# Optimization experiments

Hardware: AMD Instinct MI355X
Metric: run time of the kernel (lower is better)

Reference implementation:

```python
import jax, jax.numpy as jnp
import numpy as np


def setup_inputs() -> dict:
    key = jax.random.key(0)
    ks = jax.random.split(key, 5)
    B, S, D = 4, 2048, 1024
    x = jax.random.normal(ks[0], (B, S, D), dtype=jnp.float32)
    wq = jax.random.normal(ks[1], (D, D), dtype=jnp.float32) * (D ** -0.5)
    wk = jax.random.normal(ks[2], (D, D), dtype=jnp.float32) * (D ** -0.5)
    wv = jax.random.normal(ks[3], (D, D), dtype=jnp.float32) * (D ** -0.5)
    wo = jax.random.normal(ks[4], (D, D), dtype=jnp.float32) * (D ** -0.5)
    return {"x": x, "wq": wq, "wk": wk, "wv": wv, "wo": wo, "n_heads": 16}


def reference(x, wq, wk, wv, wo, n_heads):
    B, S, D = x.shape
    hd = D // n_heads
    # projections (module computes x @ w.T)
    q = (x @ wq.T).reshape(B, S, n_heads, hd).transpose(0, 2, 1, 3)  # b h s d
    k = (x @ wk.T).reshape(B, S, n_heads, hd).transpose(0, 2, 1, 3)
    v = (x @ wv.T).reshape(B, S, n_heads, hd).transpose(0, 2, 1, 3)
    # NOTE: module scales by sqrt(d_model), not sqrt(head_dim)
    scores = jnp.einsum("bhqd,bhkd->bhqk", q, k) / jnp.sqrt(jnp.float32(D))
    # module bug preserved: masked_fill(mask == 0, -1e9) with mask = triu(diag=1)
    # fills positions where mask is False (lower triangle incl. diagonal).
    triu_mask = jnp.triu(jnp.ones((S, S), dtype=bool), k=1)  # True strictly above diag
    scores = jnp.where(triu_mask, scores, jnp.float32(-1e9))
    attn = jax.nn.softmax(scores, axis=-1)
    out = jnp.einsum("bhqk,bhkd->bhqd", attn, v)  # b h s d
    out = out.transpose(0, 2, 1, 3).reshape(B, S, D)
    return out @ wo.T
```

## Files before the change

### kernel.cpp

```cpp
#include <hip/hip_runtime.h>
#include <hip/hip_bf16.h>

typedef __attribute__((ext_vector_type(8))) short short8;
typedef __attribute__((ext_vector_type(4))) short bfx4;
typedef __attribute__((ext_vector_type(4))) float floatx4;
typedef __attribute__((ext_vector_type(4))) __fp16 h4_t;
typedef __attribute__((ext_vector_type(2))) __fp16 h2_t;
typedef __attribute__((ext_vector_type(8))) __fp16 h8_t;

#define BATCH 4
#define SEQ 2048
#define D_MODEL 1024
#define NH 16
#define HD 64
#define ELEMS 8388608
#define WELEMS 1048576

__device__ __forceinline__ unsigned short f2bf(float f) {
    union { float f; unsigned u; } x; x.f = f;
    unsigned r = x.u + 0x7FFFu + ((x.u >> 16) & 1u);
    return (unsigned short)(r >> 16);
}
__device__ __forceinline__ unsigned short f2h(float f) {
    union { __fp16 h; unsigned short u; } x;
    x.h = (__fp16)f;
    return x.u;
}

#if __has_builtin(__builtin_amdgcn_exp2f)
__device__ __forceinline__ float fexp2(float x) { return __builtin_amdgcn_exp2f(x); }
#else
__device__ __forceinline__ float fexp2(float x) { return exp2f(x); }
#endif

__device__ __forceinline__ void gll16(const void* g, const void* l) {
    __builtin_amdgcn_global_load_lds(
        (const __attribute__((address_space(1))) void*)g,
        (__attribute__((address_space(3))) void*)l,
        16, 0, 0);
}


__global__ __launch_bounds__(256)
void cvt_kernel(const float* __restrict__ x,  const float* __restrict__ wq,
                const float* __restrict__ wk, const float* __restrict__ wv,
                const float* __restrict__ wo,
                unsigned short* __restrict__ xbf,
                unsigned short* __restrict__ wqkv,
                unsigned short* __restrict__ wobf)
{
    size_t idx = ((size_t)blockIdx.x * 256 + threadIdx.x) * 8;
    const float* src; unsigned short* dst; size_t off;
    if (idx < (size_t)ELEMS)                    { src = x;  dst = xbf;             off = idx; }
    else if (idx < (size_t)ELEMS + WELEMS)      { src = wq; dst = wqkv;            off = idx - ELEMS; }
    else if (idx < (size_t)ELEMS + 2 * WELEMS)  { src = wk; dst = wqkv + WELEMS;   off = idx - ELEMS - WELEMS; }
    else if (idx < (size_t)ELEMS + 3 * WELEMS)  { src = wv; dst = wqkv + 2*WELEMS; off = idx - ELEMS - 2*WELEMS; }
    else                                        { src = wo; dst = wobf;            off = idx - ELEMS - 3*WELEMS; }
    floatx4 a = *(const floatx4*)(src + off);
    floatx4 b = *(const floatx4*)(src + off + 4);
    short8 v;
#pragma unroll
    for (int d = 0; d < 4; d++) { v[d] = (short)f2bf(a[d]); v[4+d] = (short)f2bf(b[d]); }
    *(short8*)(dst + off) = v;
}

__global__ __launch_bounds__(256, 2)
void gemm_qkv3_kernel(const unsigned short* __restrict__ A,
                      const unsigned short* __restrict__ B,
                      unsigned short* __restrict__ Qb,
                      unsigned short* __restrict__ Kb,
                      unsigned short* __restrict__ Vb)
{
    __shared__ __align__(16) unsigned short As[128 * 64];
    __shared__ __align__(16) unsigned short Bs[128 * 64];

    const int t = threadIdx.x;
    const int wave = t >> 6, lane = t & 63;
    const int lm = lane & 15, lq = lane >> 4;
    const int wrow = (wave >> 1) * 64, wcol = (wave & 1) * 64;
    const int m0 = blockIdx.x * 128, n0 = blockIdx.y * 128;
    const int lrow = lane >> 3, lg = lane & 7;
    const int gsw = lg ^ lrow;

    floatx4 acc[4][4] = {};

    for (int k0 = 0; k0 < 1024; k0 += 64) {
        __syncthreads();
#pragma unroll
        for (int i = 0; i < 4; i++) {
            int rows8 = wave * 32 + i * 8;
            gll16(A + (size_t)(m0 + rows8 + lrow) * 1024 + k0 + gsw * 8, As + rows8 * 64);
            gll16(B + (size_t)(n0 + rows8 + lrow) * 1024 + k0 + gsw * 8, Bs + rows8 * 64);
        }
        __syncthreads();

#pragma unroll
        for (int c = 0; c < 2; c++) {
            short8 af[4], bfr[4];
#pragma unroll
            for (int i = 0; i < 4; i++) {
                int ra = wrow + i * 16 + lm;
                int g = c * 4 + lq;
                af[i] = *(const short8*)(As + (ra * 8 + (g ^ (ra & 7))) * 8);
            }
#pragma unroll
            for (int j = 0; j < 4; j++) {
                int rb = wcol + j * 16 + lm;
                int g = c * 4 + lq;
                bfr[j] = *(const short8*)(Bs + (rb * 8 + (g ^ (rb & 7))) * 8);
            }
#pragma unroll
            for (int i = 0; i < 4; i++)
#pragma unroll
                for (int j = 0; j < 4; j++)
                    acc[i][j] = __builtin_amdgcn_mfma_f32_16x16x32_bf16(
                        af[i], bfr[j], acc[i][j], 0, 0, 0);
        }
    }

    const int z = n0 >> 10;
#pragma unroll
    for (int i = 0; i < 4; i++)
#pragma unroll
        for (int j = 0; j < 4; j++)
#pragma unroll
            for (int r = 0; r < 4; r++) {
                int gm = m0 + wrow + i * 16 + lq * 4 + r;
                int gn = n0 + wcol + j * 16 + lm;
                int nl = gn & 1023, h = nl >> 6, d = nl & 63;
                int b = gm >> 11, s = gm & 2047;
                float v = acc[i][j][r];
                size_t bh = (size_t)(b * NH + h);
                if (z == 0)      Qb[(bh * SEQ + s) * HD + d] = f2bf(v);
                else if (z == 1) Kb[(bh * SEQ + s) * HD + d] = f2bf(v);
                else             Vb[(bh * HD + d) * SEQ + s] = f2h(v);
            }
}

__global__ __launch_bounds__(256, 2)
void gemm_out3_kernel(const unsigned short* __restrict__ A,
                      const unsigned short* __restrict__ B,
                      float* __restrict__ Out)
{
    __shared__ __align__(16) unsigned short As[128 * 64];
    __shared__ __align__(16) unsigned short Bs[128 * 64];

    const int t = threadIdx.x;
    const int wave = t >> 6, lane = t & 63;
    const int lm = lane & 15, lq = lane >> 4;
    const int wrow = (wave >> 1) * 64, wcol = (wave & 1) * 64;
    const int m0 = blockIdx.x * 128, n0 = blockIdx.y * 128;
    const int lrow = lane >> 3, lg = lane & 7;
    const int gsw = lg ^ lrow;

    floatx4 acc[4][4] = {};

    for (int k0 = 0; k0 < 1024; k0 += 64) {
        __syncthreads();
#pragma unroll
        for (int i = 0; i < 4; i++) {
            int rows8 = wave * 32 + i * 8;
            gll16(A + (size_t)(m0 + rows8 + lrow) * 1024 + k0 + gsw * 8, As + rows8 * 64);
            gll16(B + (size_t)(n0 + rows8 + lrow) * 1024 + k0 + gsw * 8, Bs + rows8 * 64);
        }
        __syncthreads();

#pragma unroll
        for (int c = 0; c < 2; c++) {
            short8 af[4], bfr[4];
#pragma unroll
            for (int i = 0; i < 4; i++) {
                int ra = wrow + i * 16 + lm;
                int g = c * 4 + lq;
                af[i] = *(const short8*)(As + (ra * 8 + (g ^ (ra & 7))) * 8);
            }
#pragma unroll
            for (int j = 0; j < 4; j++) {
                int rb = wcol + j * 16 + lm;
                int g = c * 4 + lq;
                bfr[j] = *(const short8*)(Bs + (rb * 8 + (g ^ (rb & 7))) * 8);
            }
#pragma unroll
            for (int i = 0; i < 4; i++)
#pragma unroll
                for (int j = 0; j < 4; j++)
                    acc[i][j] = __builtin_amdgcn_mfma_f32_16x16x32_bf16(
                        af[i], bfr[j], acc[i][j], 0, 0, 0);
        }
    }

#pragma unroll
    for (int i = 0; i < 4; i++)
#pragma unroll
        for (int j = 0; j < 4; j++)
#pragma unroll
            for (int r = 0; r < 4; r++) {
                int gm = m0 + wrow + i * 16 + lq * 4 + r;
                int gn = n0 + wcol + j * 16 + lm;
                Out[(size_t)gm * D_MODEL + gn] = acc[i][j][r];
            }
}

#define PROCESS_Q(QI, BQ, ACC, LACC, DOMASK, KT)                               \
    do {                                                                       \
        _Pragma("unroll")                                                      \
        for (int jt = 0; jt < 8; jt++) {                                       \
            floatx4 sc = {};                                                   \
            _Pragma("unroll")                                                  \
            for (int c = 0; c < 2; c++) {                                      \
                int row_ = jt * 16 + lm;                                       \
                int g_ = c * 4 + lq;                                           \
                short8 kf = *(const short8*)(Ks + (row_ * 8 + (g_ ^ (row_ & 7))) * 8); \
                sc = __builtin_amdgcn_mfma_f32_16x16x32_bf16(kf, BQ[c], sc, 0, 0, 0); \
            }                                                                  \
            if (DOMASK) {                                                      \
                _Pragma("unroll")                                              \
                for (int r = 0; r < 4; r++) {                                  \
                    int kj = (KT) * 128 + jt * 16 + lq * 4 + r;                \
                    if (!(kj > (QI))) sc[r] = -3.2e10f;                        \
                }                                                              \
            }                                                                  \
            float p0 = fexp2(sc[0] * kA), p1 = fexp2(sc[1] * kA);              \
            float p2 = fexp2(sc[2] * kA), p3 = fexp2(sc[3] * kA);              \
            LACC += (p0 + p1) + (p2 + p3);                                     \
            h2_t a01 = __builtin_amdgcn_cvt_pkrtz(p0, p1);                     \
            h2_t a23 = __builtin_amdgcn_cvt_pkrtz(p2, p3);                     \
            h4_t pf;                                                           \
            pf[0] = a01[0]; pf[1] = a01[1]; pf[2] = a23[0]; pf[3] = a23[1];    \
            _Pragma("unroll")                                                  \
            for (int jd = 0; jd < 4; jd++) {                                   \
                int rowv_ = jd * 16 + lm;                                      \
                int g16_ = jt * 2 + (lq >> 1);                                 \
                int slot_ = rowv_ * 16 + (g16_ ^ lm);                          \
                h4_t vf = *(const h4_t*)((const __fp16*)Vs + slot_ * 8 + (lq & 1) * 4); \
                ACC[jd] = __builtin_amdgcn_mfma_f32_16x16x16f16(vf, pf, ACC[jd], 0, 0, 0); \
            }                                                                  \
        }                                                                      \
    } while (0)

__global__ __launch_bounds__(256, 2)
void attn5_kernel(const unsigned short* __restrict__ Q,
                  const unsigned short* __restrict__ K,
                  const unsigned short* __restrict__ V,
                  unsigned short* __restrict__ O)
{
    __shared__ __align__(16) unsigned short Ks[128 * 64];
    __shared__ __align__(16) unsigned short Vs[64 * 128];

    const int t = threadIdx.x;
    const int wave = t >> 6, lane = t & 63;
    const int lm = lane & 15, lq = lane >> 4;
    const int bh = blockIdx.y;
    const int jlo = blockIdx.x, jhi = 31 - jlo;
    const int qlo = jlo * 64 + wave * 16 + lm;
    const int qhi = jhi * 64 + wave * 16 + lm;

    const unsigned short* Qh = Q + (size_t)bh * SEQ * HD;
    const unsigned short* Kh = K + (size_t)bh * SEQ * HD;
    const unsigned short* Vh = V + (size_t)bh * HD * SEQ;

    short8 bq_lo[2], bq_hi[2];
    bq_lo[0] = *(const short8*)(Qh + (size_t)qlo * HD + lq * 8);
    bq_lo[1] = *(const short8*)(Qh + (size_t)qlo * HD + 32 + lq * 8);
    bq_hi[0] = *(const short8*)(Qh + (size_t)qhi * HD + lq * 8);
    bq_hi[1] = *(const short8*)(Qh + (size_t)qhi * HD + 32 + lq * 8);

    floatx4 acc_lo[4] = {}, acc_hi[4] = {};
    float l_lo = 0.f, l_hi = 0.f;
    const float kA = 0.04508422002778011f;

    const int lrow = lane >> 3, lg = lane & 7;
    const int kt_min = jlo >> 1;
    const int kthi_min = 15 - kt_min;

    for (int kt = 15; kt >= kt_min; kt--) {
        __syncthreads();
#pragma unroll
        for (int i = 0; i < 4; i++) {
            int rows8 = wave * 32 + i * 8;
            gll16(Kh + (size_t)(kt * 128 + rows8 + lrow) * HD + (lg ^ lrow) * 8,
                  Ks + rows8 * 64);
        }
#pragma unroll
        for (int i = 0; i < 4; i++) {
            int rows4 = wave * 16 + i * 4;
            int row = rows4 + (lane >> 4);
            int g = (lane & 15) ^ (row & 15);
            gll16(Vh + (size_t)row * SEQ + kt * 128 + g * 8, Vs + rows4 * 128);
        }
        __syncthreads();

        PROCESS_Q(qlo, bq_lo, acc_lo, l_lo, (kt == kt_min), kt);
        if (kt >= kthi_min)
            PROCESS_Q(qhi, bq_hi, acc_hi, l_hi, (kt == kthi_min), kt);
    }

    const int b = bh >> 4, h = bh & 15;
    {
        float l = l_lo;
        l += __shfl_xor(l, 16); l += __shfl_xor(l, 32);
        float inv = 1.0f / l;
#pragma unroll
        for (int jd = 0; jd < 4; jd++) {
            bfx4 o;
#pragma unroll
            for (int r = 0; r < 4; r++) o[r] = (short)f2bf(acc_lo[jd][r] * inv);
            *(bfx4*)(O + (size_t)(b * SEQ + qlo) * D_MODEL + h * HD + jd * 16 + lq * 4) = o;
        }
    }
    {
        float l = l_hi;
        l += __shfl_xor(l, 16); l += __shfl_xor(l, 32);
        float inv = 1.0f / l;
#pragma unroll
        for (int jd = 0; jd < 4; jd++) {
            bfx4 o;
#pragma unroll
            for (int r = 0; r < 4; r++) o[r] = (short)f2bf(acc_hi[jd][r] * inv);
            *(bfx4*)(O + (size_t)(b * SEQ + qhi) * D_MODEL + h * HD + jd * 16 + lq * 4) = o;
        }
    }
}

__global__ __launch_bounds__(256, 2)
void row2047_kernel(const unsigned short* __restrict__ V,
                    unsigned short* __restrict__ O)
{
    __shared__ float red[256];
    const int bh = blockIdx.x;
    const int b = bh >> 4, h = bh & 15;
    const int t = threadIdx.x;
    const int d = t & 63, seg = t >> 6;
    const __fp16* Vh = (const __fp16*)V + (size_t)bh * HD * SEQ + (size_t)d * SEQ + seg * 512;
    float s = 0.f;
    for (int i = 0; i < 512; i += 8) {
        h8_t v = *(const h8_t*)(Vh + i);
#pragma unroll
        for (int j = 0; j < 8; j++) s += (float)v[j];
    }
    red[t] = s;
    __syncthreads();
    if (seg == 0) {
        float tot = red[d] + red[64 + d] + red[128 + d] + red[192 + d];
        O[(size_t)(b * SEQ + 2047) * D_MODEL + h * HD + d] = f2bf(tot * (1.f / 2048.f));
    }
}

__global__ __launch_bounds__(256, 2)
void gemm_qkv_kernel(const float* __restrict__ A,
                     const float* __restrict__ W0,
                     const float* __restrict__ W1,
                     const float* __restrict__ W2,
                     unsigned short* __restrict__ O0,
                     unsigned short* __restrict__ O1,
                     unsigned short* __restrict__ O2)
{
    const int K = 1024;
    const float* W;
    unsigned short* Out;
    if (blockIdx.z == 0)      { W = W0; Out = O0; }
    else if (blockIdx.z == 1) { W = W1; Out = O1; }
    else                      { W = W2; Out = O2; }

    __shared__ __align__(16) unsigned short As[128 * 64];
    __shared__ __align__(16) unsigned short Bs[128 * 64];

    const int t = threadIdx.x;
    const int wave = t >> 6, lane = t & 63;
    const int lm = lane & 15, lq = lane >> 4;
    const int wrow = (wave >> 1) * 64, wcol = (wave & 1) * 64;
    const int m0 = blockIdx.x * 128, n0 = blockIdx.y * 128;

    floatx4 acc[4][4] = {};

    for (int k0 = 0; k0 < K; k0 += 64) {
        __syncthreads();
#pragma unroll
        for (int rr = 0; rr < 4; rr++) {
            int p = rr * 256 + t;
            int row = p >> 3, g = p & 7;
            const float* pa = A + (size_t)(m0 + row) * K + k0 + g * 8;
            const float* pw = W + (size_t)(n0 + row) * K + k0 + g * 8;
            floatx4 a0 = *(const floatx4*)pa, a1 = *(const floatx4*)(pa + 4);
            floatx4 w0 = *(const floatx4*)pw, w1 = *(const floatx4*)(pw + 4);
            short8 va, vb;
#pragma unroll
            for (int d = 0; d < 4; d++) {
                va[d]     = (short)f2bf(a0[d]);
                va[4 + d] = (short)f2bf(a1[d]);
                vb[d]     = (short)f2bf(w0[d]);
                vb[4 + d] = (short)f2bf(w1[d]);
            }
            int dst = row * 8 + (g ^ (row & 7));
            *(short8*)(As + dst * 8) = va;
            *(short8*)(Bs + dst * 8) = vb;
        }
        __syncthreads();

        short8 af[4][2], bf[4][2];
#pragma unroll
        for (int i = 0; i < 4; i++)
#pragma unroll
            for (int c = 0; c < 2; c++) {
                int ra = wrow + i * 16 + lm;
                int rb = wcol + i * 16 + lm;
                int g = c * 4 + lq;
                af[i][c] = *(const short8*)(As + (ra * 8 + (g ^ (ra & 7))) * 8);
                bf[i][c] = *(const short8*)(Bs + (rb * 8 + (g ^ (rb & 7))) * 8);
            }
#pragma unroll
        for (int i = 0; i < 4; i++)
#pragma unroll
            for (int j = 0; j < 4; j++)
#pragma unroll
                for (int c = 0; c < 2; c++)
                    acc[i][j] = __builtin_amdgcn_mfma_f32_16x16x32_bf16(
                        af[i][c], bf[j][c], acc[i][j], 0, 0, 0);
    }

    const int zi = blockIdx.z;
#pragma unroll
    for (int i = 0; i < 4; i++)
#pragma unroll
        for (int j = 0; j < 4; j++)
#pragma unroll
            for (int r = 0; r < 4; r++) {
                int gm = m0 + wrow + i * 16 + lq * 4 + r;
                int gn = n0 + wcol + j * 16 + lm;
                int b = gm >> 11, s = gm & 2047;
                int h = gn >> 6, d = gn & 63;
                if (zi == 2) {
                    Out[((size_t)(b * NH + h) * HD + d) * SEQ + s] = f2h(acc[i][j][r]);
                } else {
                    Out[((size_t)(b * NH + h) * SEQ + s) * HD + d] = f2bf(acc[i][j][r]);
                }
            }
}

__global__ __launch_bounds__(256, 2)
void gemm_out_kernel(const unsigned short* __restrict__ Abf,
                     const float* __restrict__ W,
                     float* __restrict__ Out)
{
    const int K = 1024;
    __shared__ __align__(16) unsigned short As[128 * 64];
    __shared__ __align__(16) unsigned short Bs[128 * 64];

    const int t = threadIdx.x;
    const int wave = t >> 6, lane = t & 63;
    const int lm = lane & 15, lq = lane >> 4;
    const int wrow = (wave >> 1) * 64, wcol = (wave & 1) * 64;
    const int m0 = blockIdx.x * 128, n0 = blockIdx.y * 128;

    floatx4 acc[4][4] = {};

    for (int k0 = 0; k0 < K; k0 += 64) {
        __syncthreads();
#pragma unroll
        for (int rr = 0; rr < 4; rr++) {
            int p = rr * 256 + t;
            int row = p >> 3, g = p & 7;
            short8 va = *(const short8*)(Abf + (size_t)(m0 + row) * K + k0 + g * 8);
            const float* pw = W + (size_t)(n0 + row) * K + k0 + g * 8;
            floatx4 w0 = *(const floatx4*)pw, w1 = *(const floatx4*)(pw + 4);
            short8 vb;
#pragma unroll
            for (int d = 0; d < 4; d++) {
                vb[d]     = (short)f2bf(w0[d]);
                vb[4 + d] = (short)f2bf(w1[d]);
            }
            int dst = row * 8 + (g ^ (row & 7));
            *(short8*)(As + dst * 8) = va;
            *(short8*)(Bs + dst * 8) = vb;
        }
        __syncthreads();

        short8 af[4][2], bf[4][2];
#pragma unroll
        for (int i = 0; i < 4; i++)
#pragma unroll
            for (int c = 0; c < 2; c++) {
                int ra = wrow + i * 16 + lm;
                int rb = wcol + i * 16 + lm;
                int g = c * 4 + lq;
                af[i][c] = *(const short8*)(As + (ra * 8 + (g ^ (ra & 7))) * 8);
                bf[i][c] = *(const short8*)(Bs + (rb * 8 + (g ^ (rb & 7))) * 8);
            }
#pragma unroll
        for (int i = 0; i < 4; i++)
#pragma unroll
            for (int j = 0; j < 4; j++)
#pragma unroll
                for (int c = 0; c < 2; c++)
                    acc[i][j] = __builtin_amdgcn_mfma_f32_16x16x32_bf16(
                        af[i][c], bf[j][c], acc[i][j], 0, 0, 0);
    }

#pragma unroll
    for (int i = 0; i < 4; i++)
#pragma unroll
        for (int j = 0; j < 4; j++)
#pragma unroll
            for (int r = 0; r < 4; r++) {
                int gm = m0 + wrow + i * 16 + lq * 4 + r;
                int gn = n0 + wcol + j * 16 + lm;
                Out[(size_t)gm * D_MODEL + gn] = acc[i][j][r];
            }
}

extern "C" void kernel_launch(void* const* d_in, const int* in_sizes, int n_in,
                              void* d_out, int out_size, void* d_ws, size_t ws_size,
                              hipStream_t stream) {
    const float* x  = (const float*)d_in[0];
    const float* wq = (const float*)d_in[1];
    const float* wk = (const float*)d_in[2];
    const float* wv = (const float*)d_in[3];
    const float* wo = (const float*)d_in[4];

    unsigned short* ws = (unsigned short*)d_ws;
    const bool fast = ws_size >= (size_t)36 * 1024 * 1024 * 2;

    if (fast) {
        unsigned short* xbf  = ws;
        unsigned short* wqkv = ws + (size_t)ELEMS;
        unsigned short* wobf = ws + (size_t)ELEMS + 3 * WELEMS;
        unsigned short* Qb   = ws + (size_t)ELEMS + 4 * WELEMS;
        unsigned short* Kb   = Qb + ELEMS;
        unsigned short* Vb   = Kb + ELEMS;
        unsigned short* Ob   = xbf;

        cvt_kernel<<<6144, 256, 0, stream>>>(x, wq, wk, wv, wo, xbf, wqkv, wobf);
        gemm_qkv3_kernel<<<dim3(64, 24), 256, 0, stream>>>(xbf, wqkv, Qb, Kb, Vb);
        attn5_kernel<<<dim3(16, BATCH * NH), 256, 0, stream>>>(Qb, Kb, Vb, Ob);
        row2047_kernel<<<BATCH * NH, 256, 0, stream>>>(Vb, Ob);
        gemm_out3_kernel<<<dim3(64, 8), 256, 0, stream>>>(Ob, wobf, (float*)d_out);
    } else {
        unsigned short* Qb = ws;
        unsigned short* Kb = Qb + ELEMS;
        unsigned short* Vb = Kb + ELEMS;
        unsigned short* Ob = Vb + ELEMS;

        gemm_qkv_kernel<<<dim3(64, 8, 3), 256, 0, stream>>>(x, wq, wk, wv, Qb, Kb, Vb);
        attn5_kernel<<<dim3(16, BATCH * NH), 256, 0, stream>>>(Qb, Kb, Vb, Ob);
        row2047_kernel<<<BATCH * NH, 256, 0, stream>>>(Vb, Ob);
        gemm_out_kernel<<<dim3(64, 8), 256, 0, stream>>>(Ob, wo, (float*)d_out);
    }
}
```

Measured before the change: 302.3 us.

## Process two 64-row query groups per wave to reuse K/V LDS tiles

The attention kernel now gives each block 128-row query tiles instead of 64-row ones: a low tile and its mirrored high tile. Each wave computes two query row groups per tile, so every K and V fragment read from LDS feeds two MFMA chains. The grid drops from 16 to 8 blocks per head. This halves LDS traffic and global K/V loads per query, and gives more independent MFMA work between dependencies. The cost is twice the accumulator registers and half as many blocks, which lowers parallelism and load balance across CUs.

```diff
diff --git a/kernel.cpp b/kernel.cpp
--- a/kernel.cpp
+++ b/kernel.cpp
@@ -201,45 +201,68 @@
             }
 }
 
-#define PROCESS_Q(QI, BQ, ACC, LACC, DOMASK, KT)                               \
+#define PROCESS_Q2(QI0, QI1, BQ0, BQ1, ACC0, ACC1, L0, L1, DOMASK, KT)         \
     do {                                                                       \
         _Pragma("unroll")                                                      \
         for (int jt = 0; jt < 8; jt++) {                                       \
-            floatx4 sc = {};                                                   \
+            floatx4 sc0 = {}, sc1 = {};                                        \
             _Pragma("unroll")                                                  \
             for (int c = 0; c < 2; c++) {                                      \
                 int row_ = jt * 16 + lm;                                       \
                 int g_ = c * 4 + lq;                                           \
                 short8 kf = *(const short8*)(Ks + (row_ * 8 + (g_ ^ (row_ & 7))) * 8); \
-                sc = __builtin_amdgcn_mfma_f32_16x16x32_bf16(kf, BQ[c], sc, 0, 0, 0); \
+                sc0 = __builtin_amdgcn_mfma_f32_16x16x32_bf16(kf, BQ0[c], sc0, 0, 0, 0); \
+                sc1 = __builtin_amdgcn_mfma_f32_16x16x32_bf16(kf, BQ1[c], sc1, 0, 0, 0); \
             }                                                                  \
             if (DOMASK) {                                                      \
                 _Pragma("unroll")                                              \
                 for (int r = 0; r < 4; r++) {                                  \
                     int kj = (KT) * 128 + jt * 16 + lq * 4 + r;                \
-                    if (!(kj > (QI))) sc[r] = -3.2e10f;                        \
+                    if (!(kj > (QI0))) sc0[r] = -3.2e10f;                      \
+                    if (!(kj > (QI1))) sc1[r] = -3.2e10f;                      \
                 }                                                              \
             }                                                                  \
-            float p0 = fexp2(sc[0] * kA), p1 = fexp2(sc[1] * kA);              \
-            float p2 = fexp2(sc[2] * kA), p3 = fexp2(sc[3] * kA);              \
-            LACC += (p0 + p1) + (p2 + p3);                                     \
-            h2_t a01 = __builtin_amdgcn_cvt_pkrtz(p0, p1);                     \
-            h2_t a23 = __builtin_amdgcn_cvt_pkrtz(p2, p3);                     \
-            h4_t pf;                                                           \
-            pf[0] = a01[0]; pf[1] = a01[1]; pf[2] = a23[0]; pf[3] = a23[1];    \
+            float p00 = fexp2(sc0[0] * kA), p01 = fexp2(sc0[1] * kA);          \
+            float p02 = fexp2(sc0[2] * kA), p03 = fexp2(sc0[3] * kA);          \
+            float p10 = fexp2(sc1[0] * kA), p11 = fexp2(sc1[1] * kA);          \
+            float p12 = fexp2(sc1[2] * kA), p13 = fexp2(sc1[3] * kA);          \
+            L0 += (p00 + p01) + (p02 + p03);                                   \
+            L1 += (p10 + p11) + (p12 + p13);                                   \
+            h2_t a0_ = __builtin_amdgcn_cvt_pkrtz(p00, p01);                   \
+            h2_t b0_ = __builtin_amdgcn_cvt_pkrtz(p02, p03);                   \
+            h2_t a1_ = __builtin_amdgcn_cvt_pkrtz(p10, p11);                   \
+            h2_t b1_ = __builtin_amdgcn_cvt_pkrtz(p12, p13);                   \
+            h4_t pf0, pf1;                                                     \
+            pf0[0] = a0_[0]; pf0[1] = a0_[1]; pf0[2] = b0_[0]; pf0[3] = b0_[1];\
+            pf1[0] = a1_[0]; pf1[1] = a1_[1]; pf1[2] = b1_[0]; pf1[3] = b1_[1];\
             _Pragma("unroll")                                                  \
             for (int jd = 0; jd < 4; jd++) {                                   \
                 int rowv_ = jd * 16 + lm;                                      \
                 int g16_ = jt * 2 + (lq >> 1);                                 \
                 int slot_ = rowv_ * 16 + (g16_ ^ lm);                          \
                 h4_t vf = *(const h4_t*)((const __fp16*)Vs + slot_ * 8 + (lq & 1) * 4); \
-                ACC[jd] = __builtin_amdgcn_mfma_f32_16x16x16f16(vf, pf, ACC[jd], 0, 0, 0); \
+                ACC0[jd] = __builtin_amdgcn_mfma_f32_16x16x16f16(vf, pf0, ACC0[jd], 0, 0, 0); \
+                ACC1[jd] = __builtin_amdgcn_mfma_f32_16x16x16f16(vf, pf1, ACC1[jd], 0, 0, 0); \
             }                                                                  \
         }                                                                      \
     } while (0)
 
+#define WRITE_O(QROW, ACC, LV)                                                 \
+    do {                                                                       \
+        float l_ = LV;                                                         \
+        l_ += __shfl_xor(l_, 16); l_ += __shfl_xor(l_, 32);                    \
+        float inv_ = 1.0f / l_;                                                \
+        _Pragma("unroll")                                                      \
+        for (int jd = 0; jd < 4; jd++) {                                       \
+            bfx4 o_;                                                           \
+            _Pragma("unroll")                                                  \
+            for (int r = 0; r < 4; r++) o_[r] = (short)f2bf(ACC[jd][r] * inv_);\
+            *(bfx4*)(O + (size_t)(b * SEQ + (QROW)) * D_MODEL + h * HD + jd * 16 + lq * 4) = o_; \
+        }                                                                      \
+    } while (0)
+
 __global__ __launch_bounds__(256, 2)
-void attn5_kernel(const unsigned short* __restrict__ Q,
+void attn7_kernel(const unsigned short* __restrict__ Q,
                   const unsigned short* __restrict__ K,
                   const unsigned short* __restrict__ V,
                   unsigned short* __restrict__ O)
@@ -251,29 +274,34 @@
     const int wave = t >> 6, lane = t & 63;
     const int lm = lane & 15, lq = lane >> 4;
     const int bh = blockIdx.y;
-    const int jlo = blockIdx.x, jhi = 31 - jlo;
-    const int qlo = jlo * 64 + wave * 16 + lm;
-    const int qhi = jhi * 64 + wave * 16 + lm;
+    const int jlo = blockIdx.x;
+    const int ht  = 15 - jlo;
+
+    const int q_l0 = jlo * 128 + wave * 16 + lm;
+    const int q_l1 = q_l0 + 64;
+    const int q_h0 = ht * 128 + wave * 16 + lm;
+    const int q_h1 = q_h0 + 64;
 
     const unsigned short* Qh = Q + (size_t)bh * SEQ * HD;
     const unsigned short* Kh = K + (size_t)bh * SEQ * HD;
     const unsigned short* Vh = V + (size_t)bh * HD * SEQ;
 
-    short8 bq_lo[2], bq_hi[2];
-    bq_lo[0] = *(const short8*)(Qh + (size_t)qlo * HD + lq * 8);
-    bq_lo[1] = *(const short8*)(Qh + (size_t)qlo * HD + 32 + lq * 8);
-    bq_hi[0] = *(const short8*)(Qh + (size_t)qhi * HD + lq * 8);
-    bq_hi[1] = *(const short8*)(Qh + (size_t)qhi * HD + 32 + lq * 8);
-
-    floatx4 acc_lo[4] = {}, acc_hi[4] = {};
-    float l_lo = 0.f, l_hi = 0.f;
+    short8 bq_l0[2], bq_l1[2], bq_h0[2], bq_h1[2];
+#pragma unroll
+    for (int c = 0; c < 2; c++) {
+        bq_l0[c] = *(const short8*)(Qh + (size_t)q_l0 * HD + c * 32 + lq * 8);
+        bq_l1[c] = *(const short8*)(Qh + (size_t)q_l1 * HD + c * 32 + lq * 8);
+        bq_h0[c] = *(const short8*)(Qh + (size_t)q_h0 * HD + c * 32 + lq * 8);
+        bq_h1[c] = *(const short8*)(Qh + (size_t)q_h1 * HD + c * 32 + lq * 8);
+    }
+
+    floatx4 acc_l0[4] = {}, acc_l1[4] = {}, acc_h0[4] = {}, acc_h1[4] = {};
+    float l_l0 = 0.f, l_l1 = 0.f, l_h0 = 0.f, l_h1 = 0.f;
     const float kA = 0.04508422002778011f;
 
     const int lrow = lane >> 3, lg = lane & 7;
-    const int kt_min = jlo >> 1;
-    const int kthi_min = 15 - kt_min;
-
-    for (int kt = 15; kt >= kt_min; kt--) {
+
+    for (int kt = 15; kt >= jlo; kt--) {
         __syncthreads();
 #pragma unroll
         for (int i = 0; i < 4; i++) {
@@ -290,36 +318,18 @@
         }
         __syncthreads();
 
-        PROCESS_Q(qlo, bq_lo, acc_lo, l_lo, (kt == kt_min), kt);
-        if (kt >= kthi_min)
-            PROCESS_Q(qhi, bq_hi, acc_hi, l_hi, (kt == kthi_min), kt);
+        PROCESS_Q2(q_l0, q_l1, bq_l0, bq_l1, acc_l0, acc_l1, l_l0, l_l1,
+                   (kt == jlo), kt);
+        if (kt >= ht)
+            PROCESS_Q2(q_h0, q_h1, bq_h0, bq_h1, acc_h0, acc_h1, l_h0, l_h1,
+                       (kt == ht), kt);
     }
 
     const int b = bh >> 4, h = bh & 15;
-    {
-        float l = l_lo;
-        l += __shfl_xor(l, 16); l += __shfl_xor(l, 32);
-        float inv = 1.0f / l;
-#pragma unroll
-        for (int jd = 0; jd < 4; jd++) {
-            bfx4 o;
-#pragma unroll
-            for (int r = 0; r < 4; r++) o[r] = (short)f2bf(acc_lo[jd][r] * inv);
-            *(bfx4*)(O + (size_t)(b * SEQ + qlo) * D_MODEL + h * HD + jd * 16 + lq * 4) = o;
-        }
-    }
-    {
-        float l = l_hi;
-        l += __shfl_xor(l, 16); l += __shfl_xor(l, 32);
-        float inv = 1.0f / l;
-#pragma unroll
-        for (int jd = 0; jd < 4; jd++) {
-            bfx4 o;
-#pragma unroll
-            for (int r = 0; r < 4; r++) o[r] = (short)f2bf(acc_hi[jd][r] * inv);
-            *(bfx4*)(O + (size_t)(b * SEQ + qhi) * D_MODEL + h * HD + jd * 16 + lq * 4) = o;
-        }
-    }
+    WRITE_O(q_l0, acc_l0, l_l0);
+    WRITE_O(q_l1, acc_l1, l_l1);
+    WRITE_O(q_h0, acc_h0, l_h0);
+    WRITE_O(q_h1, acc_h1, l_h1);
 }
 
 __global__ __launch_bounds__(256, 2)
@@ -531,7 +541,7 @@
 
         cvt_kernel<<<6144, 256, 0, stream>>>(x, wq, wk, wv, wo, xbf, wqkv, wobf);
         gemm_qkv3_kernel<<<dim3(64, 24), 256, 0, stream>>>(xbf, wqkv, Qb, Kb, Vb);
-        attn5_kernel<<<dim3(16, BATCH * NH), 256, 0, stream>>>(Qb, Kb, Vb, Ob);
+        attn7_kernel<<<dim3(8, BATCH * NH), 256, 0, stream>>>(Qb, Kb, Vb, Ob);
         row2047_kernel<<<BATCH * NH, 256, 0, stream>>>(Vb, Ob);
         gemm_out3_kernel<<<dim3(64, 8), 256, 0, stream>>>(Ob, wobf, (float*)d_out);
     } else {
@@ -541,7 +551,7 @@
         unsigned short* Ob = Vb + ELEMS;
 
         gemm_qkv_kernel<<<dim3(64, 8, 3), 256, 0, stream>>>(x, wq, wk, wv, Qb, Kb, Vb);
-        attn5_kernel<<<dim3(16, BATCH * NH), 256, 0, stream>>>(Qb, Kb, Vb, Ob);
+        attn7_kernel<<<dim3(8, BATCH * NH), 256, 0, stream>>>(Qb, Kb, Vb, Ob);
         row2047_kernel<<<BATCH * NH, 256, 0, stream>>>(Vb, Ob);
         gemm_out_kernel<<<dim3(64, 8), 256, 0, stream>>>(Ob, wo, (float*)d_out);
     }
```

New measurement: 434.9 us. 43.9% more time.
